# Kernel optimization log

Hardware: AMD Instinct MI355X
Metric: run time of the kernel (lower is better)

Reference implementation:

```python
import jax, jax.numpy as jnp
import numpy as np

B, T, V, E, Hd, NTAG = 16, 512, 32000, 100, 500, 32
PAD, SOS, EOS = 0, 1, 2
NEG = -10000.0


def _lstm_dir(xs, mask, Wih, Whh, b, h0, c0, reverse):
    # xs: [T,B,D]; mask: [T,B] bool. Packed-sequence semantics: at padded
    # steps the state is frozen and the output is zero (pad_packed fills 0).
    def step(carry, inp):
        h, c = carry
        x_t, m = inp
        g = x_t @ Wih.T + h @ Whh.T + b
        i, f, gg, o = jnp.split(g, 4, axis=-1)  # torch gate order i,f,g,o
        c_new = jax.nn.sigmoid(f) * c + jax.nn.sigmoid(i) * jnp.tanh(gg)
        h_new = jax.nn.sigmoid(o) * jnp.tanh(c_new)
        m_ = m[:, None]
        return (jnp.where(m_, h_new, h), jnp.where(m_, c_new, c)), jnp.where(m_, h_new, 0.0)
    _, ys = jax.lax.scan(step, (h0, c0), (xs, mask), reverse=reverse)
    return ys


def _forward(x, y0, embed_W, Wih0, Whh0, bih0, bhh0, Wih1, Whh1, bih1, bhh1, W_out, b_out, trans, h0, c0):
    maskb = x > 0                       # [B,T]
    maskf = maskb.astype(embed_W.dtype)
    mT = maskb.T                        # [T,B]
    xs = embed_W[x].transpose(1, 0, 2)  # [T,B,E]
    # layer 0 (bidirectional)
    f0 = _lstm_dir(xs, mT, Wih0[0], Whh0[0], bih0[0] + bhh0[0], h0[0], c0[0], False)
    b0 = _lstm_dir(xs, mT, Wih0[1], Whh0[1], bih0[1] + bhh0[1], h0[1], c0[1], True)
    l1 = jnp.concatenate([f0, b0], axis=-1)  # [T,B,1000]
    # layer 1 (dropout omitted: deterministic reference)
    f1 = _lstm_dir(l1, mT, Wih1[0], Whh1[0], bih1[0] + bhh1[0], h0[2], c0[2], False)
    b1 = _lstm_dir(l1, mT, Wih1[1], Whh1[1], bih1[1] + bhh1[1], h0[3], c0[3], True)
    hseq = jnp.concatenate([f1, b1], axis=-1).transpose(1, 0, 2)  # [B,T,1000]
    # emissions, masked exactly as in loss(): y = y * mask
    y = (hseq @ W_out.T + b_out) * maskf[:, :, None]  # [B,T,NTAG]
    # gold path score (crf_score_batch)
    y0e = jnp.concatenate([jnp.full((B, 1), SOS, y0.dtype), y0], axis=1)
    emit = jnp.take_along_axis(y, y0e[:, 1:, None], axis=2)[..., 0]
    tr = trans[y0e[:, 1:], y0e[:, :-1]] * maskf
    gold = jnp.sum(emit + tr, axis=1)  # [B]
    # log-partition (crf_forward_batch). Faithful to the original, including
    # the quirk that finished rows are overwritten with max_g score[b,g].
    init = jnp.full((B, NTAG), NEG, y.dtype).at[:, SOS].set(0.0)
    def step(score, inp):
        emit_t, m_t = inp  # [B,NTAG], [B]
        z = score[:, None, :] + trans[None, :, :] + emit_t[:, :, None]  # [B,F,G]
        new = jax.nn.logsumexp(z, axis=2)
        carry = jnp.broadcast_to(jnp.max(score, axis=1, keepdims=True), score.shape)
        return jnp.where(m_t[:, None], new, carry), None
    final, _ = jax.lax.scan(step, init, (y.transpose(1, 0, 2), mT))
    Z = jax.nn.logsumexp(final, axis=1)
    return jnp.mean(Z - gold)


def setup_inputs() -> dict:
    key = jax.random.key(0)
    ks = jax.random.split(key, 14)
    rng = np.random.default_rng(0)
    lengths = np.sort(rng.integers(T // 4, T + 1, size=B))[::-1]  # sorted desc (pack_padded)
    valid = np.arange(T)[None, :] < lengths[:, None]
    x = rng.integers(1, V, size=(B, T)) * valid
    y0 = rng.integers(3, NTAG, size=(B, T)) * valid
    rn = lambda k, s, sc=0.1: jax.random.normal(k, s, jnp.float32) * sc
    embed_W = rn(ks[0], (V, E)).at[0].set(0.0)  # padding_idx=0
    Wih0, Whh0 = rn(ks[1], (2, 4 * Hd, E)), rn(ks[2], (2, 4 * Hd, Hd))
    bih0, bhh0 = rn(ks[3], (2, 4 * Hd)), rn(ks[4], (2, 4 * Hd))
    Wih1, Whh1 = rn(ks[5], (2, 4 * Hd, 2 * Hd)), rn(ks[6], (2, 4 * Hd, Hd))
    bih1, bhh1 = rn(ks[7], (2, 4 * Hd)), rn(ks[8], (2, 4 * Hd))
    W_out, b_out = rn(ks[9], (NTAG, 2 * Hd)), rn(ks[10], (NTAG,))
    trans = jax.random.normal(ks[11], (NTAG, NTAG), jnp.float32)
    trans = trans.at[SOS, :].set(NEG).at[:, EOS].set(NEG).at[:, PAD].set(NEG).at[PAD, :].set(NEG)
    trans = trans.at[PAD, EOS].set(0.0).at[PAD, PAD].set(0.0)
    h0 = jax.random.normal(ks[12], (4, B, Hd), jnp.float32)
    c0 = jax.random.normal(ks[13], (4, B, Hd), jnp.float32)
    return dict(x=jnp.asarray(x, jnp.int32), y0=jnp.asarray(y0, jnp.int32), embed_W=embed_W,
                Wih0=Wih0, Whh0=Whh0, bih0=bih0, bhh0=bhh0, Wih1=Wih1, Whh1=Whh1,
                bih1=bih1, bhh1=bhh1, W_out=W_out, b_out=b_out, trans=trans, h0=h0, c0=c0)


def reference(x, y0, embed_W, Wih0, Whh0, bih0, bhh0, Wih1, Whh1, bih1, bhh1, W_out, b_out, trans, h0, c0):
    return _forward(x, y0, embed_W, Wih0, Whh0, bih0, bhh0, Wih1, Whh1, bih1, bhh1, W_out, b_out, trans, h0, c0)
```

## Files before the change

### kernel.cpp

```cpp
#include <hip/hip_runtime.h>
#include <hip/hip_fp16.h>
#include <math.h>

#define TT 512
#define BB 16
#define EE 100
#define HD 500
#define NEG (-10000.0f)
#define SENT64 0xFFFFFFFFFFFFFFFFull
#define SENT32 0xFFFFFFFFu

typedef __attribute__((ext_vector_type(8))) short short8;
typedef __attribute__((ext_vector_type(4))) float f32x4;
typedef __attribute__((ext_vector_type(4))) unsigned int u32x4;
typedef __attribute__((ext_vector_type(2))) unsigned int u32x2;

__device__ inline short f2bf(float f) {
    unsigned u = __builtin_bit_cast(unsigned, f);
    unsigned r = (u + 0x7fffu + ((u >> 16) & 1u)) >> 16;
    return (short)r;
}
__device__ inline unsigned short f2h(float f) {
    __half h = __float2half(f);
    return __builtin_bit_cast(unsigned short, h);
}
__device__ inline float h2f(unsigned short u) {
    __half h = __builtin_bit_cast(__half, u);
    return __half2float(h);
}
__device__ inline float bf2f(unsigned short u) {
    return __builtin_bit_cast(float, ((unsigned)u) << 16);
}
__device__ inline float sigm_fast(float x) {
    return __builtin_amdgcn_rcpf(1.f + __expf(-x));
}
__device__ inline float tanh_fast(float x) {
    return 1.f - 2.f * __builtin_amdgcn_rcpf(__expf(2.f * x) + 1.f);
}
__device__ inline void store_u16_wt(unsigned short* p, unsigned short v) {
    asm volatile("global_store_short %0, %1, off sc0 sc1" :: "v"(p), "v"((unsigned)v) : "memory");
}

#define NSENT64B 8208
#define NEMB     4096
#define NWC0     2000
#define NWC1     16000
#define NPAD     384
__global__ __launch_bounds__(256) void prep_kernel(
    const int* __restrict__ x, int* __restrict__ mlen,
    unsigned long long* __restrict__ sentp, int* __restrict__ gcnt,
    const float* __restrict__ EW, unsigned short* __restrict__ XS,
    const float* __restrict__ Wih0, unsigned short* __restrict__ Wb0,
    const float* __restrict__ Wih1, unsigned short* __restrict__ Wb1,
    int* __restrict__ H0pad) {
    int bid = blockIdx.x;
    int tid = threadIdx.x;
    if (bid == 0) {
        __shared__ int mx;
        if (tid == 0) mx = 1;
        if (tid < 128)
            __hip_atomic_store(gcnt + tid, 0, __ATOMIC_RELAXED, __HIP_MEMORY_SCOPE_AGENT);
        __syncthreads();
        int any0 = 0, any1 = 0;
        for (int b = 0; b < BB; ++b) {
            any0 |= (x[b * TT + tid] > 0);
            any1 |= (x[b * TT + tid + 256] > 0);
        }
        if (any0) atomicMax(&mx, tid + 1);
        if (any1) atomicMax(&mx, tid + 257);
        __syncthreads();
        if (tid == 0) mlen[0] = mx;
        return;
    }
    bid -= 1;
    if (bid < NSENT64B) {
        int i = bid * 256 + tid;
        if (i < 2101248)
            __hip_atomic_store(sentp + i, SENT64, __ATOMIC_RELAXED, __HIP_MEMORY_SCOPE_AGENT);
        return;
    }
    bid -= NSENT64B;
    if (bid < NEMB) {
        int idx = bid * 256 + tid;
        int e = idx & 127;
        int r = idx >> 7;
        int t = r >> 4;
        int b = r & 15;
        unsigned short v = 0;
        if (e < EE) {
            int tok = x[b * TT + t];
            v = (unsigned short)f2bf(EW[(size_t)tok * EE + e]);
        }
        XS[idx] = v;
        return;
    }
    bid -= NEMB;
    if (bid < NWC0) {
        int i = bid * 256 + tid;
        int r = i >> 7;
        int k = i & 127;
        int z = r / 2000;
        int rl = r - z * 2000;
        int logical = (rl & 3) * 500 + (rl >> 2);
        Wb0[i] = (k < 100)
            ? (unsigned short)f2bf(Wih0[((size_t)z * 2000 + logical) * 100 + k]) : 0;
        return;
    }
    bid -= NWC0;
    if (bid < NWC1) {
        int i = bid * 256 + tid;
        int r = i >> 10;
        int k = i & 1023;
        int z = r / 2000;
        int rl = r - z * 2000;
        int logical = (rl & 3) * 500 + (rl >> 2);
        Wb1[i] = (k < 1000)
            ? (unsigned short)f2bf(Wih1[((size_t)z * 2000 + logical) * 1000 + k]) : 0;
        return;
    }
    bid -= NWC1;
    {
        int i = bid * 256 + tid;
        if (i < 8192 * 12) {
            int r = i / 12, c = i - r * 12;
            H0pad[r * 512 + 500 + c] = 0;
        }
    }
}

__global__ void sentfill_kernel(unsigned long long* __restrict__ p, int n,
                                int* __restrict__ cnt) {
    int i = blockIdx.x * 256 + threadIdx.x;
    if (i < n)
        __hip_atomic_store(p + i, SENT64, __ATOMIC_RELAXED, __HIP_MEMORY_SCOPE_AGENT);
    if (cnt && blockIdx.x == 0 && threadIdx.x < 128)
        __hip_atomic_store(cnt + threadIdx.x, 0, __ATOMIC_RELAXED, __HIP_MEMORY_SCOPE_AGENT);
}

__device__ __forceinline__ void gemm_body(
    const unsigned short* __restrict__ A, const unsigned short* __restrict__ W,
    const float* __restrict__ b1, const float* __restrict__ b2,
    unsigned short* __restrict__ C, int Kpad, int bx, int by, int z,
    int* gcnt) {
    __shared__ __align__(16) unsigned short AsS[128 * 40];
    __shared__ __align__(16) unsigned short WsS[64 * 40];
    const int tid = threadIdx.x;
    const int lane = tid & 63;
    const int w = tid >> 6;
    const int quad = lane >> 4;
    const int nl = lane & 15;
    const int bm0 = bx * 128;
    const int n0 = by * 64;

    const unsigned short* Wz = W + (size_t)z * 2000 * Kpad;
    unsigned short* Cz = C + (size_t)z * 8192 * 2000;
    const float* b1z = b1 + (size_t)z * 2000;
    const float* b2z = b2 + (size_t)z * 2000;

    f32x4 acc[2][4];
#pragma unroll
    for (int mt = 0; mt < 2; ++mt)
#pragma unroll
        for (int nt = 0; nt < 4; ++nt) acc[mt][nt] = (f32x4){0.f, 0.f, 0.f, 0.f};

    const int arow = tid >> 2;
    const int kc = tid & 3;
    const int wn = n0 + arow;
    const bool wok = (wn < 2000);

    const unsigned short* Ap0 = A + (size_t)(bm0 + arow) * Kpad + kc * 8;
    const unsigned short* Ap1 = A + (size_t)(bm0 + 64 + arow) * Kpad + kc * 8;
    const unsigned short* Wp  = Wz + (size_t)(wok ? wn : 0) * Kpad + kc * 8;

    short8 av0 = *(const short8*)(Ap0);
    short8 av1 = *(const short8*)(Ap1);
    short8 wv = {0, 0, 0, 0, 0, 0, 0, 0};
    if (wok) wv = *(const short8*)(Wp);

    for (int k0 = 0; k0 < Kpad; k0 += 32) {
        __syncthreads();
        *(short8*)&AsS[arow * 40 + kc * 8] = av0;
        *(short8*)&AsS[(64 + arow) * 40 + kc * 8] = av1;
        *(short8*)&WsS[arow * 40 + kc * 8] = wv;
        __syncthreads();

        if (k0 + 32 < Kpad) {
            av0 = *(const short8*)(Ap0 + k0 + 32);
            av1 = *(const short8*)(Ap1 + k0 + 32);
            if (wok) wv = *(const short8*)(Wp + k0 + 32);
        }

        short8 af[2], bfr[4];
#pragma unroll
        for (int mt = 0; mt < 2; ++mt)
            af[mt] = *(const short8*)&AsS[(w * 32 + mt * 16 + nl) * 40 + quad * 8];
#pragma unroll
        for (int nt = 0; nt < 4; ++nt)
            bfr[nt] = *(const short8*)&WsS[(nt * 16 + nl) * 40 + quad * 8];
#pragma unroll
        for (int mt = 0; mt < 2; ++mt)
#pragma unroll
            for (int nt = 0; nt < 4; ++nt)
                acc[mt][nt] = __builtin_amdgcn_mfma_f32_16x16x32_bf16(
                    af[mt], bfr[nt], acc[mt][nt], 0, 0, 0);
    }

#pragma unroll
    for (int nt = 0; nt < 4; ++nt) {
        int n = n0 + nt * 16 + nl;
        if (n < 2000) {
            int lg = n & 3, kk = n >> 2;
            float bb = b1z[lg * 500 + kk] + b2z[lg * 500 + kk];
#pragma unroll
            for (int mt = 0; mt < 2; ++mt) {
                int mbase = bm0 + w * 32 + mt * 16 + quad * 4;
#pragma unroll
                for (int reg = 0; reg < 4; ++reg)
                    store_u16_wt(&Cz[(size_t)(mbase + reg) * 2000 + n],
                                 f2h(acc[mt][nt][reg] + bb));
            }
        }
    }
    asm volatile("s_waitcnt vmcnt(0)" ::: "memory");
    __syncthreads();
    if (tid == 0)
        __hip_atomic_fetch_add(&gcnt[z * 64 + bx], 1,
                               __ATOMIC_RELAXED, __HIP_MEMORY_SCOPE_AGENT);
}

__device__ __forceinline__ void rec_body(
    const unsigned short* __restrict__ G, const float* __restrict__ Whh,
    const int* __restrict__ x, const float* __restrict__ h0,
    const float* __restrict__ c0, int layerbase,
    unsigned short* __restrict__ Hout, unsigned short* __restrict__ hseq,
    const int* __restrict__ mlen, int* gcnt, int blk)
{
    const int dir = blk >> 4;
    const int bsl = blk & 15;
    const int k0 = bsl * 32;
    const int tid = threadIdx.x;
    const int lane = tid & 63;
    const int w = tid >> 6;
    const int quad = lane >> 4;
    const int nl = lane & 15;
    const int L = mlen[0];

    const float* Wd = Whh + (size_t)dir * 2000 * HD;
    const unsigned short* Gd = G + (size_t)dir * TT * BB * 2000;
    unsigned short* hdir = hseq + (size_t)dir * (TT + 1) * 8192;

    __shared__ __align__(16) unsigned short hstage[8192];
    __shared__ float sg[4][32][17];

    short8 bf[2][16];
#pragma unroll
    for (int tl = 0; tl < 2; ++tl) {
        int tt = w * 2 + tl;
        int r = tt * 16 + nl;
        int g = r >> 5;
        int lkr = r & 31;
        int kk = k0 + lkr;
        const float* wrow = (kk < HD) ? (Wd + (size_t)(g * HD + kk) * HD) : (const float*)0;
#pragma unroll
        for (int ks = 0; ks < 16; ++ks) {
            int kg0 = ks * 32 + quad * 8;
            short8 v;
            if (wrow && kg0 + 8 <= HD) {
                float4 f0 = *(const float4*)(wrow + kg0);
                float4 f1 = *(const float4*)(wrow + kg0 + 4);
                v[0] = f2bf(f0.x); v[1] = f2bf(f0.y); v[2] = f2bf(f0.z); v[3] = f2bf(f0.w);
                v[4] = f2bf(f1.x); v[5] = f2bf(f1.y); v[6] = f2bf(f1.z); v[7] = f2bf(f1.w);
            } else {
#pragma unroll
                for (int j = 0; j < 8; ++j) {
                    int kg = kg0 + j;
                    float f = (wrow && kg < HD) ? wrow[kg] : 0.f;
                    v[j] = f2bf(f);
                }
            }
            bf[tl][ks] = v;
        }
    }

    const int lk = tid & 31;
    const int k  = k0 + lk;
    const bool kok = (k < HD);
    const int b0v = tid >> 5;
    const int b1v = 8 + (tid >> 5);
    float h_st[2] = {0.f, 0.f}, c_st[2] = {0.f, 0.f};
    if (kok) {
        size_t base0 = (size_t)(layerbase + dir) * BB * HD + (size_t)b0v * HD + k;
        size_t base1 = (size_t)(layerbase + dir) * BB * HD + (size_t)b1v * HD + k;
        h_st[0] = h0[base0]; c_st[0] = c0[base0];
        h_st[1] = h0[base1]; c_st[1] = c0[base1];
    }

    {
        int i0 = (int)(unsigned short)f2bf(kok ? h_st[0] : 0.f);
        int i1 = (int)(unsigned short)f2bf(kok ? h_st[1] : 0.f);
        int a0 = __shfl_down(i0, 1), c0s = __shfl_down(i0, 2), d0 = __shfl_down(i0, 3);
        int a1 = __shfl_down(i1, 1), c1s = __shfl_down(i1, 2), d1 = __shfl_down(i1, 3);
        if ((lk & 3) == 0) {
            unsigned long long p0 = (unsigned long long)(unsigned)(i0 | (a0 << 16))
                                  | ((unsigned long long)(unsigned)(c0s | (d0 << 16)) << 32);
            unsigned long long p1 = (unsigned long long)(unsigned)(i1 | (a1 << 16))
                                  | ((unsigned long long)(unsigned)(c1s | (d1 << 16)) << 32);
            int idx0 = bsl * 512 + (b0v + 16 * (lk >> 3)) * 8 + (lk & 7);
            int idx1 = bsl * 512 + (b1v + 16 * (lk >> 3)) * 8 + (lk & 7);
            __hip_atomic_store((unsigned long long*)(hdir + idx0), p0,
                               __ATOMIC_RELAXED, __HIP_MEMORY_SCOPE_AGENT);
            __hip_atomic_store((unsigned long long*)(hdir + idx1), p1,
                               __ATOMIC_RELAXED, __HIP_MEMORY_SCOPE_AGENT);
        }
    }

    u32x2 ga = {0, 0}, gb = {0, 0};
    int m[2]; m[0] = m[1] = 0;
    int lastTile = -1;

    {
        int t = dir ? (L - 1) : 0;
        if (gcnt) {
            int tile = dir * 64 + (t >> 3);
            while (__hip_atomic_load(&gcnt[tile], __ATOMIC_RELAXED,
                                     __HIP_MEMORY_SCOPE_AGENT) < 32) {}
            lastTile = tile;
        }
        if (kok) {
            const unsigned short* gr0 = Gd + ((size_t)t * BB + b0v) * 2000 + (size_t)k * 4;
            const unsigned short* gr1 = Gd + ((size_t)t * BB + b1v) * 2000 + (size_t)k * 4;
            asm volatile(
                "global_load_dwordx2 %0, %2, off sc0 sc1\n\t"
                "global_load_dwordx2 %1, %3, off sc0 sc1"
                : "=&v"(ga), "=&v"(gb) : "v"(gr0), "v"(gr1) : "memory");
            m[0] = x[b0v * TT + t] > 0;
            m[1] = x[b1v * TT + t] > 0;
        }
    }

    for (int s = 0; s < L; ++s) {
        const int t = dir ? (L - 1 - s) : s;
        const unsigned short* bufr = hdir + (size_t)s * 8192;
        unsigned short* bufw = hdir + (size_t)(s + 1) * 8192;

        {
            const unsigned short* p0 = bufr + (tid +   0) * 8;
            const unsigned short* p1 = bufr + (tid + 256) * 8;
            const unsigned short* p2 = bufr + (tid + 512) * 8;
            const unsigned short* p3 = bufr + (tid + 768) * 8;
            u32x4 c0v, c1v, c2v, c3v;
            for (;;) {
                asm volatile(
                    "global_load_dwordx4 %0, %6, off sc0 sc1\n\t"
                    "global_load_dwordx4 %1, %7, off sc0 sc1\n\t"
                    "global_load_dwordx4 %2, %8, off sc0 sc1\n\t"
                    "global_load_dwordx4 %3, %9, off sc0 sc1\n\t"
                    "s_waitcnt vmcnt(0)"
                    : "=&v"(c0v), "=&v"(c1v), "=&v"(c2v), "=&v"(c3v),
                      "+v"(ga), "+v"(gb)
                    : "v"(p0), "v"(p1), "v"(p2), "v"(p3)
                    : "memory");
                unsigned bad = 0;
#pragma unroll
                for (int q = 0; q < 4; ++q)
                    bad |= (c0v[q] == SENT32) | (c1v[q] == SENT32)
                         | (c2v[q] == SENT32) | (c3v[q] == SENT32);
                if (!bad) break;
            }
            *(u32x4*)&hstage[(tid +   0) * 8] = c0v;
            *(u32x4*)&hstage[(tid + 256) * 8] = c1v;
            *(u32x4*)&hstage[(tid + 512) * 8] = c2v;
            *(u32x4*)&hstage[(tid + 768) * 8] = c3v;
        }
        __syncthreads();

        f32x4 acc0 = {0.f, 0.f, 0.f, 0.f};
        f32x4 acc1 = {0.f, 0.f, 0.f, 0.f};
#pragma unroll
        for (int ks = 0; ks < 16; ++ks) {
            short8 a = *(const short8*)&hstage[ks * 512 + lane * 8];
            acc0 = __builtin_amdgcn_mfma_f32_16x16x32_bf16(a, bf[0][ks], acc0, 0, 0, 0);
            acc1 = __builtin_amdgcn_mfma_f32_16x16x32_bf16(a, bf[1][ks], acc1, 0, 0, 0);
        }

        {
            int r0 = (w * 2 + 0) * 16 + nl;
            int r1 = (w * 2 + 1) * 16 + nl;
            int g0r = r0 >> 5, lk0 = r0 & 31;
            int g1r = r1 >> 5, lk1 = r1 & 31;
#pragma unroll
            for (int reg = 0; reg < 4; ++reg) {
                int b = quad * 4 + reg;
                sg[g0r][lk0][b] = acc0[reg];
                sg[g1r][lk1][b] = acc1[reg];
            }
        }
        __syncthreads();

        int i0 = 0, i1 = 0;
        if (kok) {
            {
                unsigned w0 = ga[0], w1 = ga[1];
                float si  = sg[0][lk][b0v] + h2f((unsigned short)(w0 & 0xffffu));
                float sf  = sg[1][lk][b0v] + h2f((unsigned short)(w0 >> 16));
                float sgg = sg[2][lk][b0v] + h2f((unsigned short)(w1 & 0xffffu));
                float so  = sg[3][lk][b0v] + h2f((unsigned short)(w1 >> 16));
                float c_new = sigm_fast(sf) * c_st[0] + sigm_fast(si) * tanh_fast(sgg);
                float h_new = sigm_fast(so) * tanh_fast(c_new);
                if (m[0]) { h_st[0] = h_new; c_st[0] = c_new; }
            }
            {
                unsigned w0 = gb[0], w1 = gb[1];
                float si  = sg[0][lk][b1v] + h2f((unsigned short)(w0 & 0xffffu));
                float sf  = sg[1][lk][b1v] + h2f((unsigned short)(w0 >> 16));
                float sgg = sg[2][lk][b1v] + h2f((unsigned short)(w1 & 0xffffu));
                float so  = sg[3][lk][b1v] + h2f((unsigned short)(w1 >> 16));
                float c_new = sigm_fast(sf) * c_st[1] + sigm_fast(si) * tanh_fast(sgg);
                float h_new = sigm_fast(so) * tanh_fast(c_new);
                if (m[1]) { h_st[1] = h_new; c_st[1] = c_new; }
            }
            i0 = (int)(unsigned short)f2bf(h_st[0]);
            i1 = (int)(unsigned short)f2bf(h_st[1]);
        }

        {
            int a0 = __shfl_down(i0, 1), c0s = __shfl_down(i0, 2), d0 = __shfl_down(i0, 3);
            int a1 = __shfl_down(i1, 1), c1s = __shfl_down(i1, 2), d1 = __shfl_down(i1, 3);
            if ((lk & 3) == 0) {
                unsigned long long p0 = (unsigned long long)(unsigned)(i0 | (a0 << 16))
                                      | ((unsigned long long)(unsigned)(c0s | (d0 << 16)) << 32);
                unsigned long long p1 = (unsigned long long)(unsigned)(i1 | (a1 << 16))
                                      | ((unsigned long long)(unsigned)(c1s | (d1 << 16)) << 32);
                int idx0 = bsl * 512 + (b0v + 16 * (lk >> 3)) * 8 + (lk & 7);
                int idx1 = bsl * 512 + (b1v + 16 * (lk >> 3)) * 8 + (lk & 7);
                __hip_atomic_store((unsigned long long*)(bufw + idx0), p0,
                                   __ATOMIC_RELAXED, __HIP_MEMORY_SCOPE_AGENT);
                __hip_atomic_store((unsigned long long*)(bufw + idx1), p1,
                                   __ATOMIC_RELAXED, __HIP_MEMORY_SCOPE_AGENT);
            }
        }

        if (kok) {
            Hout[((size_t)t * BB + b0v) * 1024 + dir * HD + k] =
                (unsigned short)(m[0] ? i0 : 0);
            Hout[((size_t)t * BB + b1v) * 1024 + dir * HD + k] =
                (unsigned short)(m[1] ? i1 : 0);
        }

        if (s + 1 < L) {
            int tn = dir ? (L - 2 - s) : (s + 1);
            if (gcnt) {
                int tile = dir * 64 + (tn >> 3);
                if (tile != lastTile) {
                    while (__hip_atomic_load(&gcnt[tile], __ATOMIC_RELAXED,
                                             __HIP_MEMORY_SCOPE_AGENT) < 32) {}
                    lastTile = tile;
                }
            }
            if (kok) {
                const unsigned short* gr0 = Gd + ((size_t)tn * BB + b0v) * 2000 + (size_t)k * 4;
                const unsigned short* gr1 = Gd + ((size_t)tn * BB + b1v) * 2000 + (size_t)k * 4;
                asm volatile(
                    "global_load_dwordx2 %0, %2, off sc0 sc1\n\t"
                    "global_load_dwordx2 %1, %3, off sc0 sc1"
                    : "=&v"(ga), "=&v"(gb) : "v"(gr0), "v"(gr1) : "memory");
                m[0] = x[b0v * TT + tn] > 0;
                m[1] = x[b1v * TT + tn] > 0;
            }
        }
    }
}

__global__ __launch_bounds__(256, 1) void fused_kernel(
    const unsigned short* __restrict__ A, const unsigned short* __restrict__ Wb,
    const float* __restrict__ b1, const float* __restrict__ b2,
    unsigned short* __restrict__ Gh, int Kpad,
    const float* __restrict__ Whh, const int* __restrict__ x,
    const float* __restrict__ h0, const float* __restrict__ c0, int layerbase,
    unsigned short* __restrict__ Hout, unsigned short* __restrict__ hseq,
    const int* __restrict__ mlen, int* gcnt) {
    int bid = blockIdx.x;
    if (bid < 32) {
        rec_body(Gh, Whh, x, h0, c0, layerbase, Hout, hseq, mlen, gcnt, bid);
    } else {
        int gx = bid - 32;
        int z = gx & 1;
        int rem = gx >> 1;
        int bx = rem >> 5;
        int by = rem & 31;
        if (z) bx = 63 - bx;
        gemm_body(A, Wb, b1, b2, Gh, Kpad, bx, by, z, gcnt);
    }
}

__global__ __launch_bounds__(256) void outproj_kernel(
    const unsigned short* __restrict__ HS, const float* __restrict__ Wo,
    const float* __restrict__ bo, const int* __restrict__ x,
    float* __restrict__ Y) {
    __shared__ float wlds[8 * 1000];
    const int bid = blockIdx.x;
    const int tid = threadIdx.x;
    const int rblk = bid >> 2;
    const int n0 = (bid & 3) * 8;
    for (int i = tid; i < 8000; i += 256) {
        int nn = i / 1000;
        int q = i - nn * 1000;
        wlds[i] = Wo[(size_t)(n0 + nn) * 1000 + q];
    }
    __syncthreads();
    const int r = rblk * 32 + (tid >> 3);
    const int n = n0 + (tid & 7);
    const int t = r >> 4;
    const int b = r & 15;
    float out = 0.f;
    if (x[b * TT + t] > 0) {
        const unsigned short* h = HS + (size_t)r * 1024;
        const float* wrow = &wlds[(tid & 7) * 1000];
        float s = 0.f;
#pragma unroll 4
        for (int q = 0; q < 1000; q += 8) {
            short8 hv = *(const short8*)(h + q);
            float4 w0 = *(const float4*)(wrow + q);
            float4 w1 = *(const float4*)(wrow + q + 4);
            s += bf2f((unsigned short)hv[0]) * w0.x + bf2f((unsigned short)hv[1]) * w0.y
               + bf2f((unsigned short)hv[2]) * w0.z + bf2f((unsigned short)hv[3]) * w0.w
               + bf2f((unsigned short)hv[4]) * w1.x + bf2f((unsigned short)hv[5]) * w1.y
               + bf2f((unsigned short)hv[6]) * w1.z + bf2f((unsigned short)hv[7]) * w1.w;
        }
        out = s + bo[n];
    }
    Y[(size_t)r * 32 + n] = out;
}

__global__ __launch_bounds__(1024) void crf_kernel(
    const float* __restrict__ Y, const int* __restrict__ x, const int* __restrict__ y0,
    const float* __restrict__ trans, float* __restrict__ out_pb) {
    int b = blockIdx.x;
    int tid = threadIdx.x;
    int i = tid >> 5;
    int j = tid & 31;
    float tr_ij = trans[i * 32 + j];

    __shared__ float scb[2][32];
    __shared__ float wred[16];
    __shared__ float goldS;

    float gp = 0.f;
    if (tid < TT) {
        int t = tid;
        int xm = x[b * TT + t];
        float mf = (xm > 0) ? 1.f : 0.f;
        int ynext = y0[b * TT + t];
        int yprev = (t == 0) ? 1 : y0[b * TT + t - 1];
        gp = Y[((size_t)t * BB + b) * 32 + ynext] + trans[ynext * 32 + yprev] * mf;
    }
#pragma unroll
    for (int d = 32; d >= 1; d >>= 1) gp += __shfl_down(gp, d);
    if ((tid & 63) == 0) wred[tid >> 6] = gp;
    __syncthreads();
    if (tid == 0) {
        float s = 0.f;
        for (int ww = 0; ww < 16; ++ww) s += wred[ww];
        goldS = s;
    }
    if (tid < 32) scb[0][tid] = (tid == 1) ? 0.f : NEG;
    __syncthreads();

    int cur = 0;
    float emit_c = Y[((size_t)0 * BB + b) * 32 + i];
    int mm_c = x[b * TT + 0] > 0;
    for (int t = 0; t < TT; ++t) {
        float emit_n = 0.f;
        int mm_n = 0;
        if (t + 1 < TT) {
            emit_n = Y[((size_t)(t + 1) * BB + b) * 32 + i];
            mm_n = x[b * TT + t + 1] > 0;
        }
        float sj = scb[cur][j];
        float z = sj + tr_ij;
        float mx = z;
#pragma unroll
        for (int d = 16; d >= 1; d >>= 1) mx = fmaxf(mx, __shfl_xor(mx, d));
        float e = __expf(z - mx);
#pragma unroll
        for (int d = 16; d >= 1; d >>= 1) e += __shfl_xor(e, d);
        float cm = sj;
#pragma unroll
        for (int d = 16; d >= 1; d >>= 1) cm = fmaxf(cm, __shfl_xor(cm, d));
        float newv = emit_c + mx + __logf(e);
        if (j == 0) scb[cur ^ 1][i] = mm_c ? newv : cm;
        __syncthreads();
        cur ^= 1;
        emit_c = emit_n;
        mm_c = mm_n;
    }

    if (tid < 32) {
        float v = scb[cur][tid];
        float mx = v;
#pragma unroll
        for (int d = 16; d >= 1; d >>= 1) mx = fmaxf(mx, __shfl_xor(mx, d));
        float e = __expf(v - mx);
#pragma unroll
        for (int d = 16; d >= 1; d >>= 1) e += __shfl_xor(e, d);
        if (tid == 0) out_pb[b] = (mx + __logf(e)) - goldS;
    }
}

__global__ void final_kernel(const float* __restrict__ out_pb, float* __restrict__ out) {
    if (threadIdx.x == 0 && blockIdx.x == 0) {
        float s = 0.f;
        for (int b = 0; b < BB; ++b) s += out_pb[b];
        out[0] = s / (float)BB;
    }
}

extern "C" void kernel_launch(void* const* d_in, const int* in_sizes, int n_in,
                              void* d_out, int out_size, void* d_ws, size_t ws_size,
                              hipStream_t stream) {
    const int*   x     = (const int*)d_in[0];
    const int*   y0    = (const int*)d_in[1];
    const float* EW    = (const float*)d_in[2];
    const float* Wih0  = (const float*)d_in[3];
    const float* Whh0  = (const float*)d_in[4];
    const float* bih0  = (const float*)d_in[5];
    const float* bhh0  = (const float*)d_in[6];
    const float* Wih1  = (const float*)d_in[7];
    const float* Whh1  = (const float*)d_in[8];
    const float* bih1  = (const float*)d_in[9];
    const float* bhh1  = (const float*)d_in[10];
    const float* Wo    = (const float*)d_in[11];
    const float* bo    = (const float*)d_in[12];
    const float* trans = (const float*)d_in[13];
    const float* h0    = (const float*)d_in[14];
    const float* c0    = (const float*)d_in[15];

    float* ws = (float*)d_ws;
    unsigned short* XS = (unsigned short*)ws;
    float* Y      = ws;
    float* crfbuf = ws + 262144;
    unsigned short* Gh   = (unsigned short*)(ws + 524288);
    unsigned short* H0b  = (unsigned short*)(ws + 16908288);
    unsigned short* HSb  = (unsigned short*)(ws + 21102592);
    unsigned short* Wb0  = (unsigned short*)(ws + 25296896);
    unsigned short* Wb1  = (unsigned short*)(ws + 25552896);
    unsigned short* hseq = (unsigned short*)(ws + 27600896);
    int* mlen     = (int*)(ws + 31803392);
    int* gcnt     = (int*)(ws + 31803393);
    const int nsent64 = 2 * (TT + 1) * 8192 / 4;

    const int nprep = 1 + NSENT64B + NEMB + NWC0 + NWC1 + NPAD;
    prep_kernel<<<nprep, 256, 0, stream>>>(x, mlen, (unsigned long long*)hseq, gcnt,
                                           EW, XS, Wih0, Wb0, Wih1, Wb1, (int*)H0b);

    fused_kernel<<<32 + 4096, 256, 0, stream>>>(XS, Wb0, bih0, bhh0, Gh, 128,
                                                Whh0, x, h0, c0, 0, H0b, hseq, mlen, gcnt);

    sentfill_kernel<<<(nsent64 + 255) / 256, 256, 0, stream>>>((unsigned long long*)hseq, nsent64, gcnt);

    fused_kernel<<<32 + 4096, 256, 0, stream>>>(H0b, Wb1, bih1, bhh1, Gh, 1024,
                                                Whh1, x, h0, c0, 2, HSb, hseq, mlen, gcnt);

    outproj_kernel<<<1024, 256, 0, stream>>>(HSb, Wo, bo, x, Y);

    crf_kernel<<<BB, 1024, 0, stream>>>(Y, x, y0, trans, crfbuf);

    final_kernel<<<1, 64, 0, stream>>>(crfbuf, (float*)d_out);
}
```

Before: 2.615 ms.

## Overlap layer-1 weight conversion, vectorize sentinel fill, single-wave CRF with fused final

Moves the layer-1 input-weight bf16 conversion out of the prep kernel into extra blocks of the layer-0 fused kernel, so it runs alongside the recurrence. Sentinel fills now use 16-byte stores instead of 8-byte atomics. The CRF kernel is rewritten to one 64-lane wave per batch row that keeps transition rows in registers, avoids block barriers, and stops early at the first padded step. The separate final-reduction kernel is folded in through an atomic counter. The extra conversion blocks may compete with the recurrence blocks for resources, and the early break depends on masks being contiguous prefixes.

Result: faster. 2.393 ms (-8.5%).

```diff
diff --git a/kernel.cpp b/kernel.cpp
--- a/kernel.cpp
+++ b/kernel.cpp
@@ -40,25 +40,27 @@
 __device__ inline void store_u16_wt(unsigned short* p, unsigned short v) {
     asm volatile("global_store_short %0, %1, off sc0 sc1" :: "v"(p), "v"((unsigned)v) : "memory");
 }
-
-#define NSENT64B 8208
+__device__ inline void store_sent16(void* p) {
+    u32x4 s = {SENT32, SENT32, SENT32, SENT32};
+    asm volatile("global_store_dwordx4 %0, %1, off sc0 sc1" :: "v"(p), "v"(s) : "memory");
+}
+
+#define NSENTB   4104
 #define NEMB     4096
 #define NWC0     2000
-#define NWC1     16000
 #define NPAD     384
 __global__ __launch_bounds__(256) void prep_kernel(
     const int* __restrict__ x, int* __restrict__ mlen,
     unsigned long long* __restrict__ sentp, int* __restrict__ gcnt,
     const float* __restrict__ EW, unsigned short* __restrict__ XS,
     const float* __restrict__ Wih0, unsigned short* __restrict__ Wb0,
-    const float* __restrict__ Wih1, unsigned short* __restrict__ Wb1,
     int* __restrict__ H0pad) {
     int bid = blockIdx.x;
     int tid = threadIdx.x;
     if (bid == 0) {
         __shared__ int mx;
         if (tid == 0) mx = 1;
-        if (tid < 128)
+        if (tid < 132)
             __hip_atomic_store(gcnt + tid, 0, __ATOMIC_RELAXED, __HIP_MEMORY_SCOPE_AGENT);
         __syncthreads();
         int any0 = 0, any1 = 0;
@@ -73,13 +75,12 @@
         return;
     }
     bid -= 1;
-    if (bid < NSENT64B) {
+    if (bid < NSENTB) {
         int i = bid * 256 + tid;
-        if (i < 2101248)
-            __hip_atomic_store(sentp + i, SENT64, __ATOMIC_RELAXED, __HIP_MEMORY_SCOPE_AGENT);
+        store_sent16((char*)sentp + (size_t)i * 16);
         return;
     }
-    bid -= NSENT64B;
+    bid -= NSENTB;
     if (bid < NEMB) {
         int idx = bid * 256 + tid;
         int e = idx & 127;
@@ -107,18 +108,6 @@
         return;
     }
     bid -= NWC0;
-    if (bid < NWC1) {
-        int i = bid * 256 + tid;
-        int r = i >> 10;
-        int k = i & 1023;
-        int z = r / 2000;
-        int rl = r - z * 2000;
-        int logical = (rl & 3) * 500 + (rl >> 2);
-        Wb1[i] = (k < 1000)
-            ? (unsigned short)f2bf(Wih1[((size_t)z * 2000 + logical) * 1000 + k]) : 0;
-        return;
-    }
-    bid -= NWC1;
     {
         int i = bid * 256 + tid;
         if (i < 8192 * 12) {
@@ -128,12 +117,12 @@
     }
 }
 
-__global__ void sentfill_kernel(unsigned long long* __restrict__ p, int n,
+__global__ void sentfill_kernel(unsigned long long* __restrict__ p, int n16,
                                 int* __restrict__ cnt) {
     int i = blockIdx.x * 256 + threadIdx.x;
-    if (i < n)
-        __hip_atomic_store(p + i, SENT64, __ATOMIC_RELAXED, __HIP_MEMORY_SCOPE_AGENT);
-    if (cnt && blockIdx.x == 0 && threadIdx.x < 128)
+    if (i < n16)
+        store_sent16((char*)p + (size_t)i * 16);
+    if (cnt && blockIdx.x == 0 && threadIdx.x < 132)
         __hip_atomic_store(cnt + threadIdx.x, 0, __ATOMIC_RELAXED, __HIP_MEMORY_SCOPE_AGENT);
 }
 
@@ -478,11 +467,12 @@
     const float* __restrict__ Whh, const int* __restrict__ x,
     const float* __restrict__ h0, const float* __restrict__ c0, int layerbase,
     unsigned short* __restrict__ Hout, unsigned short* __restrict__ hseq,
-    const int* __restrict__ mlen, int* gcnt) {
+    const int* __restrict__ mlen, int* gcnt,
+    const float* __restrict__ Wc_src, unsigned short* __restrict__ Wc_dst) {
     int bid = blockIdx.x;
     if (bid < 32) {
         rec_body(Gh, Whh, x, h0, c0, layerbase, Hout, hseq, mlen, gcnt, bid);
-    } else {
+    } else if (bid < 32 + 4096) {
         int gx = bid - 32;
         int z = gx & 1;
         int rem = gx >> 1;
@@ -490,6 +480,15 @@
         int by = rem & 31;
         if (z) bx = 63 - bx;
         gemm_body(A, Wb, b1, b2, Gh, Kpad, bx, by, z, gcnt);
+    } else {
+        int i = (bid - 4128) * 256 + threadIdx.x;
+        int r = i >> 10;
+        int k = i & 1023;
+        int z = r / 2000;
+        int rl = r - z * 2000;
+        int logical = (rl & 3) * 500 + (rl >> 2);
+        Wc_dst[i] = (k < 1000)
+            ? (unsigned short)f2bf(Wc_src[((size_t)z * 2000 + logical) * 1000 + k]) : 0;
     }
 }
 
@@ -532,42 +531,35 @@
     Y[(size_t)r * 32 + n] = out;
 }
 
-__global__ __launch_bounds__(1024) void crf_kernel(
+__global__ __launch_bounds__(64) void crf_kernel(
     const float* __restrict__ Y, const int* __restrict__ x, const int* __restrict__ y0,
-    const float* __restrict__ trans, float* __restrict__ out_pb) {
-    int b = blockIdx.x;
-    int tid = threadIdx.x;
-    int i = tid >> 5;
-    int j = tid & 31;
-    float tr_ij = trans[i * 32 + j];
-
-    __shared__ float scb[2][32];
-    __shared__ float wred[16];
-    __shared__ float goldS;
+    const float* __restrict__ trans, float* __restrict__ out_pb,
+    float* __restrict__ out, int* __restrict__ fcnt) {
+    const int b = blockIdx.x;
+    const int lane = threadIdx.x;
+    const int i = lane & 31;
+    const int half = lane >> 5;
+    __shared__ float sc[32];
+
+    float tr[16];
+#pragma unroll
+    for (int jj = 0; jj < 16; ++jj) tr[jj] = trans[i * 32 + half * 16 + jj];
 
     float gp = 0.f;
-    if (tid < TT) {
-        int t = tid;
+    for (int t = lane; t < TT; t += 64) {
         int xm = x[b * TT + t];
         float mf = (xm > 0) ? 1.f : 0.f;
         int ynext = y0[b * TT + t];
         int yprev = (t == 0) ? 1 : y0[b * TT + t - 1];
-        gp = Y[((size_t)t * BB + b) * 32 + ynext] + trans[ynext * 32 + yprev] * mf;
+        gp += Y[((size_t)t * BB + b) * 32 + ynext] + trans[ynext * 32 + yprev] * mf;
     }
 #pragma unroll
     for (int d = 32; d >= 1; d >>= 1) gp += __shfl_down(gp, d);
-    if ((tid & 63) == 0) wred[tid >> 6] = gp;
-    __syncthreads();
-    if (tid == 0) {
-        float s = 0.f;
-        for (int ww = 0; ww < 16; ++ww) s += wred[ww];
-        goldS = s;
-    }
-    if (tid < 32) scb[0][tid] = (tid == 1) ? 0.f : NEG;
-    __syncthreads();
-
-    int cur = 0;
-    float emit_c = Y[((size_t)0 * BB + b) * 32 + i];
+    float goldS = __shfl(gp, 0);
+
+    if (half == 0) sc[i] = (i == 1) ? 0.f : NEG;
+
+    float emit_c = Y[(size_t)b * 32 + i];
     int mm_c = x[b * TT + 0] > 0;
     for (int t = 0; t < TT; ++t) {
         float emit_n = 0.f;
@@ -576,42 +568,60 @@
             emit_n = Y[((size_t)(t + 1) * BB + b) * 32 + i];
             mm_n = x[b * TT + t + 1] > 0;
         }
-        float sj = scb[cur][j];
-        float z = sj + tr_ij;
-        float mx = z;
-#pragma unroll
-        for (int d = 16; d >= 1; d >>= 1) mx = fmaxf(mx, __shfl_xor(mx, d));
-        float e = __expf(z - mx);
-#pragma unroll
-        for (int d = 16; d >= 1; d >>= 1) e += __shfl_xor(e, d);
-        float cm = sj;
-#pragma unroll
-        for (int d = 16; d >= 1; d >>= 1) cm = fmaxf(cm, __shfl_xor(cm, d));
-        float newv = emit_c + mx + __logf(e);
-        if (j == 0) scb[cur ^ 1][i] = mm_c ? newv : cm;
-        __syncthreads();
-        cur ^= 1;
+        const float* sch = &sc[half * 16];
+        float4 s0 = *(const float4*)(sch + 0);
+        float4 s1 = *(const float4*)(sch + 4);
+        float4 s2 = *(const float4*)(sch + 8);
+        float4 s3 = *(const float4*)(sch + 12);
+        float sj[16] = {s0.x, s0.y, s0.z, s0.w, s1.x, s1.y, s1.z, s1.w,
+                        s2.x, s2.y, s2.z, s2.w, s3.x, s3.y, s3.z, s3.w};
+        if (mm_c) {
+            float z[16];
+#pragma unroll
+            for (int jj = 0; jj < 16; ++jj) z[jj] = sj[jj] + tr[jj];
+            float m1 = z[0];
+#pragma unroll
+            for (int jj = 1; jj < 16; ++jj) m1 = fmaxf(m1, z[jj]);
+            float mx = fmaxf(m1, __shfl_xor(m1, 32));
+            float e1 = 0.f;
+#pragma unroll
+            for (int jj = 0; jj < 16; ++jj) e1 += __expf(z[jj] - mx);
+            float et = e1 + __shfl_xor(e1, 32);
+            float newv = emit_c + mx + __logf(et);
+            if (half == 0) sc[i] = newv;
+        } else {
+            float c1 = sj[0];
+#pragma unroll
+            for (int jj = 1; jj < 16; ++jj) c1 = fmaxf(c1, sj[jj]);
+            float cm = fmaxf(c1, __shfl_xor(c1, 32));
+            if (half == 0) sc[i] = cm;
+            break;
+        }
         emit_c = emit_n;
         mm_c = mm_n;
     }
 
-    if (tid < 32) {
-        float v = scb[cur][tid];
-        float mx = v;
-#pragma unroll
-        for (int d = 16; d >= 1; d >>= 1) mx = fmaxf(mx, __shfl_xor(mx, d));
-        float e = __expf(v - mx);
-#pragma unroll
-        for (int d = 16; d >= 1; d >>= 1) e += __shfl_xor(e, d);
-        if (tid == 0) out_pb[b] = (mx + __logf(e)) - goldS;
-    }
-}
-
-__global__ void final_kernel(const float* __restrict__ out_pb, float* __restrict__ out) {
-    if (threadIdx.x == 0 && blockIdx.x == 0) {
-        float s = 0.f;
-        for (int b = 0; b < BB; ++b) s += out_pb[b];
-        out[0] = s / (float)BB;
+    float v = sc[i];
+    float mx = v;
+#pragma unroll
+    for (int d = 16; d >= 1; d >>= 1) mx = fmaxf(mx, __shfl_xor(mx, d));
+    float e = __expf(v - mx);
+#pragma unroll
+    for (int d = 16; d >= 1; d >>= 1) e += __shfl_xor(e, d);
+
+    if (lane == 0) {
+        float zb = (mx + __logf(e)) - goldS;
+        __hip_atomic_store(&out_pb[b], zb, __ATOMIC_RELAXED, __HIP_MEMORY_SCOPE_AGENT);
+        asm volatile("s_waitcnt vmcnt(0)" ::: "memory");
+        int old = __hip_atomic_fetch_add(fcnt, 1, __ATOMIC_RELAXED,
+                                         __HIP_MEMORY_SCOPE_AGENT);
+        if (old == BB - 1) {
+            float s = 0.f;
+            for (int bb = 0; bb < BB; ++bb)
+                s += __hip_atomic_load(&out_pb[bb], __ATOMIC_RELAXED,
+                                       __HIP_MEMORY_SCOPE_AGENT);
+            out[0] = s / (float)BB;
+        }
     }
 }
 
@@ -647,23 +657,24 @@
     unsigned short* hseq = (unsigned short*)(ws + 27600896);
     int* mlen     = (int*)(ws + 31803392);
     int* gcnt     = (int*)(ws + 31803393);
-    const int nsent64 = 2 * (TT + 1) * 8192 / 4;
-
-    const int nprep = 1 + NSENT64B + NEMB + NWC0 + NWC1 + NPAD;
+    int* fcnt     = gcnt + 128;
+    const int nsent16 = 2 * (TT + 1) * 8192 / 8;
+
+    const int nprep = 1 + NSENTB + NEMB + NWC0 + NPAD;
     prep_kernel<<<nprep, 256, 0, stream>>>(x, mlen, (unsigned long long*)hseq, gcnt,
-                                           EW, XS, Wih0, Wb0, Wih1, Wb1, (int*)H0b);
-
-    fused_kernel<<<32 + 4096, 256, 0, stream>>>(XS, Wb0, bih0, bhh0, Gh, 128,
-                                                Whh0, x, h0, c0, 0, H0b, hseq, mlen, gcnt);
-
-    sentfill_kernel<<<(nsent64 + 255) / 256, 256, 0, stream>>>((unsigned long long*)hseq, nsent64, gcnt);
-
-    fused_kernel<<<32 + 4096, 256, 0, stream>>>(H0b, Wb1, bih1, bhh1, Gh, 1024,
-                                                Whh1, x, h0, c0, 2, HSb, hseq, mlen, gcnt);
+                                           EW, XS, Wih0, Wb0, (int*)H0b);
+
+    fused_kernel<<<32 + 4096 + 16000, 256, 0, stream>>>(
+        XS, Wb0, bih0, bhh0, Gh, 128, Whh0, x, h0, c0, 0, H0b, hseq, mlen, gcnt,
+        Wih1, Wb1);
+
+    sentfill_kernel<<<NSENTB, 256, 0, stream>>>((unsigned long long*)hseq, nsent16, gcnt);
+
+    fused_kernel<<<32 + 4096, 256, 0, stream>>>(
+        H0b, Wb1, bih1, bhh1, Gh, 1024, Whh1, x, h0, c0, 2, HSb, hseq, mlen, gcnt,
+        nullptr, nullptr);
 
     outproj_kernel<<<1024, 256, 0, stream>>>(HSb, Wo, bo, x, Y);
 
-    crf_kernel<<<BB, 1024, 0, stream>>>(Y, x, y0, trans, crfbuf);
-
-    final_kernel<<<1, 64, 0, stream>>>(crfbuf, (float*)d_out);
-}
+    crf_kernel<<<BB, 64, 0, stream>>>(Y, x, y0, trans, crfbuf, (float*)d_out, fcnt);
+}
```
